# Performance work log

Hardware: AMD Instinct MI355X
Metric: run time of the kernel (lower is better)

Reference implementation:

```python
import jax, jax.numpy as jnp
import numpy as np

HEAD_NUM = 16
HIDDEN = 1024
HEAD_DIM = HIDDEN // HEAD_NUM


def setup_inputs() -> dict:
    key = jax.random.key(0)
    ks = jax.random.split(key, 9)
    B, S, D = 1, 4096, HIDDEN
    scale = 1.0 / np.sqrt(D)
    inp = {
        "x": jax.random.normal(ks[0], (B, S, D), jnp.float32),
        "wq": jax.random.normal(ks[1], (D, D), jnp.float32) * scale,
        "bq": jnp.zeros((D,), jnp.float32),
        "wk": jax.random.normal(ks[2], (D, D), jnp.float32) * scale,
        "bk": jnp.zeros((D,), jnp.float32),
        "wv": jax.random.normal(ks[3], (D, D), jnp.float32) * scale,
        "bv": jnp.zeros((D,), jnp.float32),
        "wo": jax.random.normal(ks[4], (D, D), jnp.float32) * scale,
        "bo": jnp.zeros((D,), jnp.float32),
    }
    return inp


def reference(x, wq, bq, wk, bk, wv, bv, wo, bo):
    B, S, D = x.shape
    H, Hd = HEAD_NUM, HEAD_DIM
    # QKV projections (weights stored as [in, out])
    q = (x @ wq + bq).reshape(B, S, H, Hd).transpose(0, 2, 1, 3)  # [B,H,S,Hd]
    k = (x @ wk + bk).reshape(B, S, H, Hd).transpose(0, 2, 1, 3)
    v = (x @ wv + bv).reshape(B, S, H, Hd).transpose(0, 2, 1, 3)
    scores = jnp.einsum("bhqd,bhkd->bhqk", q, k) / jnp.sqrt(jnp.float32(Hd))
    attn = jax.nn.softmax(scores, axis=-1)  # dropout in eval mode = identity
    out = jnp.einsum("bhqk,bhkd->bhqd", attn, v)
    out = out.transpose(0, 2, 1, 3).reshape(B, S, D)
    return out @ wo + bo
```

## Files before the change

kernel.cpp:

```cpp
#include <hip/hip_runtime.h>

#define S_LEN  4096
#define DMODEL 1024
#define NHEAD  16
#define HDIM   64

typedef unsigned short u16;
typedef unsigned int   u32;
typedef __bf16 bf16x8 __attribute__((ext_vector_type(8)));
typedef float  f32x4  __attribute__((ext_vector_type(4)));

static __device__ __forceinline__ u16 f2b(float f) {
    union { __bf16 b; u16 u; } c; c.b = (__bf16)f; return c.u;
}

typedef __attribute__((address_space(3))) u32 lds_u32_t;
typedef __attribute__((address_space(1))) const u32 glb_u32_t;
static __device__ __forceinline__ void gload_lds16(const u16* g, u16* l) {
    __builtin_amdgcn_global_load_lds((glb_u32_t*)g, (lds_u32_t*)l, 16, 0, 0);
}

__global__ __launch_bounds__(256)
void convert_x(const float* __restrict__ x, u16* __restrict__ xb) {
    const int i0 = (blockIdx.x * 256 + threadIdx.x) * 8;
    float4 a = *reinterpret_cast<const float4*>(x + i0);
    float4 b = *reinterpret_cast<const float4*>(x + i0 + 4);
    u16 o[8] = {f2b(a.x), f2b(a.y), f2b(a.z), f2b(a.w),
                f2b(b.x), f2b(b.y), f2b(b.z), f2b(b.w)};
    *reinterpret_cast<uint4*>(xb + i0) = *reinterpret_cast<uint4*>(o);
}

__global__ __launch_bounds__(256)
void transpose_w(const float* __restrict__ w, u16* __restrict__ wT) {
    const int k0 = blockIdx.x * 64, n0 = blockIdx.y * 64;
    const int t = threadIdx.x;
    __shared__ u16 T[64][72];
    const int kk = t >> 4, nn = (t & 15) * 4;
    #pragma unroll
    for (int i = 0; i < 4; ++i) {
        float4 v = *reinterpret_cast<const float4*>(w + (size_t)(k0 + kk + i * 16) * DMODEL + n0 + nn);
        T[nn + 0][kk + i * 16] = f2b(v.x);
        T[nn + 1][kk + i * 16] = f2b(v.y);
        T[nn + 2][kk + i * 16] = f2b(v.z);
        T[nn + 3][kk + i * 16] = f2b(v.w);
    }
    __syncthreads();
    const int n = t >> 2, kc = (t & 3) * 16;
    uint4 r0 = *reinterpret_cast<const uint4*>(&T[n][kc]);
    uint4 r1 = *reinterpret_cast<const uint4*>(&T[n][kc + 8]);
    u16* dst = wT + (size_t)(n0 + n) * DMODEL + k0 + kc;
    *reinterpret_cast<uint4*>(dst)     = r0;
    *reinterpret_cast<uint4*>(dst + 8) = r1;
}

template<int MODE>
__global__ __launch_bounds__(256, 2)
void gemm128(const u16* __restrict__ A, const u16* __restrict__ BT,
             const float* __restrict__ b0, const float* __restrict__ b1,
             const float* __restrict__ b2, void* __restrict__ Cout) {
    const int m0 = blockIdx.x * 128;
    const int ny = blockIdx.y;
    const int tz = (MODE == 0) ? (ny >> 3) : 0;
    const int n0 = (MODE == 0) ? ((ny & 7) * 128) : (ny * 128);
    const int tid = threadIdx.x, lane = tid & 63, w = tid >> 6;
    const int wr = w >> 1, wc = w & 1;
    const int fm = lane & 15, fq = lane >> 4;

    __shared__ u16 As[128][32];
    __shared__ u16 Bs[128][32];

    const u16* Bb = BT + (size_t)tz * DMODEL * DMODEL;

    f32x4 acc[4][4];
    #pragma unroll
    for (int i = 0; i < 4; ++i)
        #pragma unroll
        for (int t = 0; t < 4; ++t) acc[i][t] = f32x4{0.f, 0.f, 0.f, 0.f};

    const int srow = lane >> 2, scol = (lane & 3) * 8;

    for (int k0 = 0; k0 < DMODEL; k0 += 32) {
        #pragma unroll
        for (int r = 0; r < 2; ++r) {
            const int rowA = w * 32 + r * 16;
            gload_lds16(A  + (size_t)(m0 + rowA + srow) * DMODEL + k0 + scol, &As[rowA][0]);
            gload_lds16(Bb + (size_t)(n0 + rowA + srow) * DMODEL + k0 + scol, &Bs[rowA][0]);
        }
        __syncthreads();
        bf16x8 af[4], bf[4];
        #pragma unroll
        for (int i = 0; i < 4; ++i) af[i] = *reinterpret_cast<const bf16x8*>(&As[wr * 64 + i * 16 + fm][fq * 8]);
        #pragma unroll
        for (int t = 0; t < 4; ++t) bf[t] = *reinterpret_cast<const bf16x8*>(&Bs[wc * 64 + t * 16 + fm][fq * 8]);
        #pragma unroll
        for (int i = 0; i < 4; ++i)
            #pragma unroll
            for (int t = 0; t < 4; ++t)
                acc[i][t] = __builtin_amdgcn_mfma_f32_16x16x32_bf16(af[i], bf[t], acc[i][t], 0, 0, 0);
        __syncthreads();
    }

    const float* bp = (MODE == 0) ? ((tz == 0) ? b0 : (tz == 1) ? b1 : b2) : b0;
    #pragma unroll
    for (int t = 0; t < 4; ++t) {
        const int col = n0 + wc * 64 + t * 16 + fm;
        const float bias = bp[col];
        #pragma unroll
        for (int i = 0; i < 4; ++i) {
            #pragma unroll
            for (int r = 0; r < 4; ++r) {
                const int row = m0 + wr * 64 + i * 16 + fq * 4 + r;
                const float v = acc[i][t][r] + bias;
                if (MODE == 0) {
                    const int hh = col >> 6, d = col & 63;
                    ((u16*)Cout)[(size_t)tz * S_LEN * DMODEL + ((size_t)hh * S_LEN + row) * HDIM + d] = f2b(v);
                } else {
                    ((float*)Cout)[(size_t)row * DMODEL + col] = v;
                }
            }
        }
    }
}

__global__ __launch_bounds__(256, 2)
void attn_kernel(const u16* __restrict__ Q, const u16* __restrict__ K,
                 const u16* __restrict__ V, u16* __restrict__ O) {
    const int qt = blockIdx.x, h = blockIdx.y;
    const int tid = threadIdx.x, lane = tid & 63, wid = tid >> 6;
    const int fm = lane & 15, fq = lane >> 4;

    __shared__ __bf16 Ps[128][72];
    __shared__ u16 Ks[2][64][72];
    __shared__ u16 Vt[2][64][72];

    const u16* Qh = Q + (size_t)h * S_LEN * HDIM;
    const u16* Kh = K + (size_t)h * S_LEN * HDIM;
    const u16* Vh = V + (size_t)h * S_LEN * HDIM;

    const int srow = tid >> 2, sch = (tid & 3) * 16;
    const int kp = tid & 31, vg = (tid >> 5) * 8;

    bf16x8 qf[2][2];
    #pragma unroll
    for (int rb = 0; rb < 2; ++rb) {
        const u16* qsrc = Qh + (size_t)(qt * 128 + wid * 32 + rb * 16 + fm) * HDIM + fq * 8;
        qf[rb][0] = *reinterpret_cast<const bf16x8*>(qsrc);
        qf[rb][1] = *reinterpret_cast<const bf16x8*>(qsrc + 32);
    }

    float rsum[2][4] = {{0.f,0.f,0.f,0.f},{0.f,0.f,0.f,0.f}};
    f32x4 oacc[2][4];
    #pragma unroll
    for (int rb = 0; rb < 2; ++rb)
        #pragma unroll
        for (int t = 0; t < 4; ++t) oacc[rb][t] = f32x4{0.f, 0.f, 0.f, 0.f};

    uint4 kr0, kr1, vr0, vr1;
    {
        const u16* ks = Kh + (size_t)srow * HDIM + sch;
        kr0 = *reinterpret_cast<const uint4*>(ks);
        kr1 = *reinterpret_cast<const uint4*>(ks + 8);
        const u16* vs = Vh + (size_t)(2 * kp) * HDIM + vg;
        vr0 = *reinterpret_cast<const uint4*>(vs);
        vr1 = *reinterpret_cast<const uint4*>(vs + HDIM);
    }

    for (int kt = 0; kt < S_LEN / 64; ++kt) {
        const int p = kt & 1;
        *reinterpret_cast<uint4*>(&Ks[p][srow][sch])     = kr0;
        *reinterpret_cast<uint4*>(&Ks[p][srow][sch + 8]) = kr1;
        {
            union { uint4 q; u16 hw[8]; } a, b;
            a.q = vr0; b.q = vr1;
            #pragma unroll
            for (int j = 0; j < 8; ++j) {
                u32 pk = (u32)a.hw[j] | ((u32)b.hw[j] << 16);
                *reinterpret_cast<u32*>(&Vt[p][vg + j][2 * kp]) = pk;
            }
        }
        __syncthreads();

        if (kt + 1 < S_LEN / 64) {
            const u16* ks = Kh + (size_t)((kt + 1) * 64 + srow) * HDIM + sch;
            kr0 = *reinterpret_cast<const uint4*>(ks);
            kr1 = *reinterpret_cast<const uint4*>(ks + 8);
            const u16* vs = Vh + (size_t)((kt + 1) * 64 + 2 * kp) * HDIM + vg;
            vr0 = *reinterpret_cast<const uint4*>(vs);
            vr1 = *reinterpret_cast<const uint4*>(vs + HDIM);
        }

        f32x4 sacc[2][4];
        #pragma unroll
        for (int rb = 0; rb < 2; ++rb)
            #pragma unroll
            for (int t = 0; t < 4; ++t) sacc[rb][t] = f32x4{0.f, 0.f, 0.f, 0.f};
        #pragma unroll
        for (int kk2 = 0; kk2 < 2; ++kk2) {
            #pragma unroll
            for (int t = 0; t < 4; ++t) {
                bf16x8 bf = *reinterpret_cast<const bf16x8*>(&Ks[p][t * 16 + fm][kk2 * 32 + fq * 8]);
                #pragma unroll
                for (int rb = 0; rb < 2; ++rb)
                    sacc[rb][t] = __builtin_amdgcn_mfma_f32_16x16x32_bf16(qf[rb][kk2], bf, sacc[rb][t], 0, 0, 0);
            }
        }

        #pragma unroll
        for (int rb = 0; rb < 2; ++rb) {
            #pragma unroll
            for (int t = 0; t < 4; ++t) {
                #pragma unroll
                for (int r = 0; r < 4; ++r) {
                    float e = __expf(sacc[rb][t][r] * 0.125f);
                    rsum[rb][r] += e;
                    Ps[wid * 32 + rb * 16 + fq * 4 + r][t * 16 + fm] = (__bf16)e;
                }
            }
        }

        #pragma unroll
        for (int kk2 = 0; kk2 < 2; ++kk2) {
            bf16x8 af[2];
            #pragma unroll
            for (int rb = 0; rb < 2; ++rb)
                af[rb] = *reinterpret_cast<const bf16x8*>(&Ps[wid * 32 + rb * 16 + fm][kk2 * 32 + fq * 8]);
            #pragma unroll
            for (int t = 0; t < 4; ++t) {
                bf16x8 bf = *reinterpret_cast<const bf16x8*>(&Vt[p][t * 16 + fm][kk2 * 32 + fq * 8]);
                #pragma unroll
                for (int rb = 0; rb < 2; ++rb)
                    oacc[rb][t] = __builtin_amdgcn_mfma_f32_16x16x32_bf16(af[rb], bf, oacc[rb][t], 0, 0, 0);
            }
        }
    }

    float l[2][4];
    #pragma unroll
    for (int rb = 0; rb < 2; ++rb)
        #pragma unroll
        for (int r = 0; r < 4; ++r) {
            float rs = rsum[rb][r];
            #pragma unroll
            for (int m = 1; m < 16; m <<= 1) rs += __shfl_xor(rs, m, 64);
            l[rb][r] = rs;
        }

    #pragma unroll
    for (int rb = 0; rb < 2; ++rb)
        #pragma unroll
        for (int t = 0; t < 4; ++t) {
            const int d = t * 16 + fm;
            #pragma unroll
            for (int r = 0; r < 4; ++r) {
                const int row = qt * 128 + wid * 32 + rb * 16 + fq * 4 + r;
                O[(size_t)row * DMODEL + h * HDIM + d] = f2b(oacc[rb][t][r] / l[rb][r]);
            }
        }
}

extern "C" void kernel_launch(void* const* d_in, const int* in_sizes, int n_in,
                              void* d_out, int out_size, void* d_ws, size_t ws_size,
                              hipStream_t stream) {
    const float* x  = (const float*)d_in[0];
    const float* wq = (const float*)d_in[1];
    const float* bq = (const float*)d_in[2];
    const float* wk = (const float*)d_in[3];
    const float* bk = (const float*)d_in[4];
    const float* wv = (const float*)d_in[5];
    const float* bv = (const float*)d_in[6];
    const float* wo = (const float*)d_in[7];
    const float* bo = (const float*)d_in[8];

    u16* ws = (u16*)d_ws;
    const size_t MW  = (size_t)DMODEL * DMODEL;
    const size_t NX  = (size_t)S_LEN * DMODEL;
    const size_t TSZ = (size_t)NHEAD * S_LEN * HDIM;

    u16* xb = ws;
    u16* WT = xb + NX;
    u16* Qb = WT + 4 * MW;
    u16* Ob = Qb + 3 * TSZ;

    hipLaunchKernelGGL(convert_x, dim3(NX / 2048), dim3(256), 0, stream, x, xb);
    hipLaunchKernelGGL(transpose_w, dim3(16, 16), dim3(256), 0, stream, wq, WT);
    hipLaunchKernelGGL(transpose_w, dim3(16, 16), dim3(256), 0, stream, wk, WT + MW);
    hipLaunchKernelGGL(transpose_w, dim3(16, 16), dim3(256), 0, stream, wv, WT + 2 * MW);
    hipLaunchKernelGGL(transpose_w, dim3(16, 16), dim3(256), 0, stream, wo, WT + 3 * MW);

    hipLaunchKernelGGL((gemm128<0>), dim3(S_LEN / 128, 24), dim3(256), 0, stream,
                       xb, WT, bq, bk, bv, (void*)Qb);
    hipLaunchKernelGGL(attn_kernel, dim3(S_LEN / 128, NHEAD), dim3(256), 0, stream,
                       Qb, Qb + TSZ, Qb + 2 * TSZ, Ob);
    hipLaunchKernelGGL((gemm128<1>), dim3(S_LEN / 128, 8), dim3(256), 0, stream,
                       Ob, WT + 3 * MW, bo, bo, bo, d_out);
}
```

Before: 277.1 us.

## Transpose score MFMA to write P rows contiguously and merge weight transposes

The QK^T MFMA operands are swapped so each lane holds four consecutive key positions for one query row. The exp'd probabilities can then be written to LDS as packed 64-bit stores instead of scattered 16-bit stores, and the row sum reduces to two shuffles plus a broadcast. LDS row padding shrinks from 72 to 68 and the launch bound allows three blocks per CU, trading register budget for occupancy. The four weight-transpose launches are merged into one 3D-grid launch to cut launch overhead.

```diff
diff --git a/kernel.cpp b/kernel.cpp
--- a/kernel.cpp
+++ b/kernel.cpp
@@ -31,7 +31,12 @@
 }
 
 __global__ __launch_bounds__(256)
-void transpose_w(const float* __restrict__ w, u16* __restrict__ wT) {
+void transpose_w4(const float* __restrict__ w0, const float* __restrict__ w1,
+                  const float* __restrict__ w2, const float* __restrict__ w3,
+                  u16* __restrict__ wT) {
+    const int z = blockIdx.z;
+    const float* w = (z == 0) ? w0 : (z == 1) ? w1 : (z == 2) ? w2 : w3;
+    u16* dst0 = wT + (size_t)z * DMODEL * DMODEL;
     const int k0 = blockIdx.x * 64, n0 = blockIdx.y * 64;
     const int t = threadIdx.x;
     __shared__ u16 T[64][72];
@@ -48,7 +53,7 @@
     const int n = t >> 2, kc = (t & 3) * 16;
     uint4 r0 = *reinterpret_cast<const uint4*>(&T[n][kc]);
     uint4 r1 = *reinterpret_cast<const uint4*>(&T[n][kc + 8]);
-    u16* dst = wT + (size_t)(n0 + n) * DMODEL + k0 + kc;
+    u16* dst = dst0 + (size_t)(n0 + n) * DMODEL + k0 + kc;
     *reinterpret_cast<uint4*>(dst)     = r0;
     *reinterpret_cast<uint4*>(dst + 8) = r1;
 }
@@ -122,16 +127,16 @@
     }
 }
 
-__global__ __launch_bounds__(256, 2)
+__global__ __launch_bounds__(256, 3)
 void attn_kernel(const u16* __restrict__ Q, const u16* __restrict__ K,
                  const u16* __restrict__ V, u16* __restrict__ O) {
     const int qt = blockIdx.x, h = blockIdx.y;
     const int tid = threadIdx.x, lane = tid & 63, wid = tid >> 6;
     const int fm = lane & 15, fq = lane >> 4;
 
-    __shared__ __bf16 Ps[128][72];
-    __shared__ u16 Ks[2][64][72];
-    __shared__ u16 Vt[2][64][72];
+    __shared__ alignas(16) u16 Pt[128][68];
+    __shared__ alignas(16) u16 Ks[2][64][68];
+    __shared__ alignas(16) u16 Vt[2][64][68];
 
     const u16* Qh = Q + (size_t)h * S_LEN * HDIM;
     const u16* Kh = K + (size_t)h * S_LEN * HDIM;
@@ -148,7 +153,7 @@
         qf[rb][1] = *reinterpret_cast<const bf16x8*>(qsrc + 32);
     }
 
-    float rsum[2][4] = {{0.f,0.f,0.f,0.f},{0.f,0.f,0.f,0.f}};
+    float rsum[2] = {0.f, 0.f};
     f32x4 oacc[2][4];
     #pragma unroll
     for (int rb = 0; rb < 2; ++rb)
@@ -193,28 +198,32 @@
         #pragma unroll
         for (int rb = 0; rb < 2; ++rb)
             #pragma unroll
-            for (int t = 0; t < 4; ++t) sacc[rb][t] = f32x4{0.f, 0.f, 0.f, 0.f};
+            for (int mt = 0; mt < 4; ++mt) sacc[rb][mt] = f32x4{0.f, 0.f, 0.f, 0.f};
         #pragma unroll
         for (int kk2 = 0; kk2 < 2; ++kk2) {
             #pragma unroll
-            for (int t = 0; t < 4; ++t) {
-                bf16x8 bf = *reinterpret_cast<const bf16x8*>(&Ks[p][t * 16 + fm][kk2 * 32 + fq * 8]);
+            for (int mt = 0; mt < 4; ++mt) {
+                bf16x8 kf = *reinterpret_cast<const bf16x8*>(&Ks[p][mt * 16 + fm][kk2 * 32 + fq * 8]);
                 #pragma unroll
                 for (int rb = 0; rb < 2; ++rb)
-                    sacc[rb][t] = __builtin_amdgcn_mfma_f32_16x16x32_bf16(qf[rb][kk2], bf, sacc[rb][t], 0, 0, 0);
+                    sacc[rb][mt] = __builtin_amdgcn_mfma_f32_16x16x32_bf16(kf, qf[rb][kk2], sacc[rb][mt], 0, 0, 0);
             }
         }
 
         #pragma unroll
         for (int rb = 0; rb < 2; ++rb) {
             #pragma unroll
-            for (int t = 0; t < 4; ++t) {
-                #pragma unroll
-                for (int r = 0; r < 4; ++r) {
-                    float e = __expf(sacc[rb][t][r] * 0.125f);
-                    rsum[rb][r] += e;
-                    Ps[wid * 32 + rb * 16 + fq * 4 + r][t * 16 + fm] = (__bf16)e;
-                }
+            for (int mt = 0; mt < 4; ++mt) {
+                u32 pk[2];
+                float e0 = __expf(sacc[rb][mt][0] * 0.125f);
+                float e1 = __expf(sacc[rb][mt][1] * 0.125f);
+                float e2 = __expf(sacc[rb][mt][2] * 0.125f);
+                float e3 = __expf(sacc[rb][mt][3] * 0.125f);
+                rsum[rb] += (e0 + e1) + (e2 + e3);
+                pk[0] = (u32)f2b(e0) | ((u32)f2b(e1) << 16);
+                pk[1] = (u32)f2b(e2) | ((u32)f2b(e3) << 16);
+                *reinterpret_cast<uint2*>(&Pt[wid * 32 + rb * 16 + fm][mt * 16 + fq * 4]) =
+                    uint2{pk[0], pk[1]};
             }
         }
 
@@ -223,7 +232,7 @@
             bf16x8 af[2];
             #pragma unroll
             for (int rb = 0; rb < 2; ++rb)
-                af[rb] = *reinterpret_cast<const bf16x8*>(&Ps[wid * 32 + rb * 16 + fm][kk2 * 32 + fq * 8]);
+                af[rb] = *reinterpret_cast<const bf16x8*>(&Pt[wid * 32 + rb * 16 + fm][kk2 * 32 + fq * 8]);
             #pragma unroll
             for (int t = 0; t < 4; ++t) {
                 bf16x8 bf = *reinterpret_cast<const bf16x8*>(&Vt[p][t * 16 + fm][kk2 * 32 + fq * 8]);
@@ -236,14 +245,13 @@
 
     float l[2][4];
     #pragma unroll
-    for (int rb = 0; rb < 2; ++rb)
-        #pragma unroll
-        for (int r = 0; r < 4; ++r) {
-            float rs = rsum[rb][r];
-            #pragma unroll
-            for (int m = 1; m < 16; m <<= 1) rs += __shfl_xor(rs, m, 64);
-            l[rb][r] = rs;
-        }
+    for (int rb = 0; rb < 2; ++rb) {
+        float rs = rsum[rb];
+        rs += __shfl_xor(rs, 16, 64);
+        rs += __shfl_xor(rs, 32, 64);
+        #pragma unroll
+        for (int r = 0; r < 4; ++r) l[rb][r] = __shfl(rs, fq * 4 + r, 64);
+    }
 
     #pragma unroll
     for (int rb = 0; rb < 2; ++rb)
@@ -282,10 +290,7 @@
     u16* Ob = Qb + 3 * TSZ;
 
     hipLaunchKernelGGL(convert_x, dim3(NX / 2048), dim3(256), 0, stream, x, xb);
-    hipLaunchKernelGGL(transpose_w, dim3(16, 16), dim3(256), 0, stream, wq, WT);
-    hipLaunchKernelGGL(transpose_w, dim3(16, 16), dim3(256), 0, stream, wk, WT + MW);
-    hipLaunchKernelGGL(transpose_w, dim3(16, 16), dim3(256), 0, stream, wv, WT + 2 * MW);
-    hipLaunchKernelGGL(transpose_w, dim3(16, 16), dim3(256), 0, stream, wo, WT + 3 * MW);
+    hipLaunchKernelGGL(transpose_w4, dim3(16, 16, 4), dim3(256), 0, stream, wq, wk, wv, wo, WT);
 
     hipLaunchKernelGGL((gemm128<0>), dim3(S_LEN / 128, 24), dim3(256), 0, stream,
                        xb, WT, bq, bk, bv, (void*)Qb);
```

Result: faster. 263.5 us (-4.9%).
